# Optimization experiments

Hardware: AMD Instinct MI355X
Metric: run time of the kernel (lower is better)

The kernel has to match this reference:

```python
import jax, jax.numpy as jnp
import numpy as np

N_NODES = 50000
N_EDGES = 800000
IN_CH = 128
HEADS = 2
OUT_CH = 64


def setup_inputs() -> dict:
    key = jax.random.key(0)
    k1, k2, k3, k4, k5 = jax.random.split(key, 5)
    x = jax.random.normal(k1, (N_NODES, IN_CH), dtype=jnp.float32)
    W = jax.random.normal(k2, (IN_CH, HEADS * OUT_CH), dtype=jnp.float32) / np.sqrt(IN_CH)
    att_src = jax.random.normal(k3, (HEADS, OUT_CH), dtype=jnp.float32) / np.sqrt(OUT_CH)
    att_dst = jax.random.normal(k4, (HEADS, OUT_CH), dtype=jnp.float32) / np.sqrt(OUT_CH)
    bias = jnp.zeros((OUT_CH,), dtype=jnp.float32)
    edge_index = jax.random.randint(k5, (2, N_EDGES), 0, N_NODES, dtype=jnp.int64)
    return {"x": x, "W": W, "att_src": att_src, "att_dst": att_dst,
            "bias": bias, "edge_index": edge_index}


def reference(x, W, att_src, att_dst, bias, edge_index):
    # PyG GATConv forward (heads=2, concat=False, add_self_loops=True,
    # negative_slope=0.2, bias on mean-over-heads output).
    N = x.shape[0]
    H, C = att_src.shape
    h = (x @ W).reshape(N, H, C)                       # [N, H, C] projected features

    loop = jnp.arange(N, dtype=edge_index.dtype)
    src = jnp.concatenate([edge_index[0], loop])        # [E+N] message sources
    dst = jnp.concatenate([edge_index[1], loop])        # [E+N] softmax segments

    # per-node attention halves, then gather scalars per edge
    a_src = jnp.einsum('nhc,hc->nh', h, att_src)        # [N, H]
    a_dst = jnp.einsum('nhc,hc->nh', h, att_dst)        # [N, H]
    e = jax.nn.leaky_relu(a_src[src] + a_dst[dst], 0.2) # [E+N, H]

    # segment-softmax over incoming edges of each destination node
    e_max = jax.ops.segment_max(e, dst, num_segments=N)            # [N, H]
    e_exp = jnp.exp(e - e_max[dst])                                 # [E+N, H]
    denom = jax.ops.segment_sum(e_exp, dst, num_segments=N)         # [N, H] (>0: self-loops)
    alpha = e_exp / denom[dst]                                      # [E+N, H]

    # weighted scatter-add aggregation
    msg = alpha[:, :, None] * h[src]                                # [E+N, H, C]
    out = jax.ops.segment_sum(msg, dst, num_segments=N)             # [N, H, C]
    return out.mean(axis=1) + bias                                  # concat=False -> head mean
```

## Files before the change

### kernel.cpp

```cpp
#include <hip/hip_runtime.h>

#define NN 50000
#define NE 800000
#define ETOT (NE + NN)
#define INCH 128
#define OUTC 64
#define LOG2E 1.44269504088896f
#define NBK 196
#define BCAP 5120
#define EPB 1024
#define BTH 1024

#define OFF_HBUF  0
#define OFF_ASRC  12800000
#define OFF_ADST  13200000
#define OFF_GBC   13600000
#define OFF_BBASE 13601024
#define OFF_OFF   13602048
#define OFF_SRC16 13802052
#define OFF_WPK   15502052
#define OFF_BINB  18902052

typedef __attribute__((ext_vector_type(8))) short short8v;
typedef __attribute__((ext_vector_type(4))) float float4v;
typedef unsigned long long ull;

__device__ __forceinline__ unsigned short f2bf(float f) {
    unsigned u = __float_as_uint(f);
    u += 0x7fffu + ((u >> 16) & 1u);
    return (unsigned short)(u >> 16);
}
__device__ __forceinline__ unsigned packbf(float a, float b) {
    return (unsigned)f2bf(a) | ((unsigned)f2bf(b) << 16);
}

#define PITCH 272
#define XLDS_BYTES (64 * PITCH)
#define WT_OFF XLDS_BYTES
#define SMEM_BYTES (XLDS_BYTES + 128 * PITCH)

__global__ __launch_bounds__(256) void k_proj(const float* __restrict__ x,
                                              const float* __restrict__ W,
                                              const float* __restrict__ att_src,
                                              const float* __restrict__ att_dst,
                                              unsigned* __restrict__ hbuf,
                                              float2* __restrict__ asrc,
                                              float2* __restrict__ adst) {
    __shared__ char smem[SMEM_BYTES];
    const int t = threadIdx.x;
    const int nbase = blockIdx.x * 64;

    {
        const int rl = t >> 2;
        const int q  = t & 3;
        int rg = nbase + rl;
        if (rg >= NN) rg = NN - 1;
        const float4* src = (const float4*)(x + (size_t)rg * INCH + q * 32);
        char* dst = smem + rl * PITCH + q * 64;
#pragma unroll
        for (int i = 0; i < 8; ++i) {
            const float4 v = src[i];
            const unsigned lo = packbf(v.x, v.y);
            const unsigned hi = packbf(v.z, v.w);
            *(ull*)(dst + i * 8) = (ull)lo | ((ull)hi << 32);
        }
    }
    {
        const int c  = t & 127;
        const int kh = t >> 7;
        const float* wcol = W + c;
        char* dst = smem + WT_OFF + c * PITCH + kh * 128;
#pragma unroll
        for (int i = 0; i < 16; ++i) {
            const int k = kh * 64 + i * 4;
            const float w0 = wcol[(size_t)(k + 0) * 128];
            const float w1 = wcol[(size_t)(k + 1) * 128];
            const float w2 = wcol[(size_t)(k + 2) * 128];
            const float w3 = wcol[(size_t)(k + 3) * 128];
            const unsigned lo = packbf(w0, w1);
            const unsigned hi = packbf(w2, w3);
            *(ull*)(dst + i * 8) = (ull)lo | ((ull)hi << 32);
        }
    }
    __syncthreads();

    const int w  = t >> 6;
    const int l  = t & 63;
    const int li = l & 15;
    const int g  = l >> 4;

    const char* xb = smem + (w * 16 + li) * PITCH + g * 16;
    const char* wb = smem + WT_OFF + li * PITCH + g * 16;

    float4v acc[8] = {};
#pragma unroll
    for (int ks = 0; ks < 4; ++ks) {
        const short8v aF = *(const short8v*)(xb + ks * 64);
#pragma unroll
        for (int nt = 0; nt < 8; ++nt) {
            const short8v bF = *(const short8v*)(wb + nt * (16 * PITCH) + ks * 64);
            acc[nt] = __builtin_amdgcn_mfma_f32_16x16x32_bf16(aF, bF, acc[nt], 0, 0, 0);
        }
    }

    float aS0[4], aS1[4], aD0[4], aD1[4];
#pragma unroll
    for (int tt = 0; tt < 4; ++tt) {
        aS0[tt] = att_src[tt * 16 + li];
        aS1[tt] = att_src[64 + tt * 16 + li];
        aD0[tt] = att_dst[tt * 16 + li];
        aD1[tt] = att_dst[64 + tt * 16 + li];
    }
#pragma unroll
    for (int r = 0; r < 4; ++r) {
        const int n = nbase + w * 16 + g * 4 + r;
        const bool valid = (n < NN);
        float ps0 = 0.f, ps1 = 0.f, pd0 = 0.f, pd1 = 0.f;
#pragma unroll
        for (int tt = 0; tt < 4; ++tt) {
            const float h0 = acc[tt][r];
            const float h1 = acc[tt + 4][r];
            if (valid) hbuf[(size_t)n * 64 + tt * 16 + li] = packbf(h0, h1);
            ps0 += h0 * aS0[tt];
            ps1 += h1 * aS1[tt];
            pd0 += h0 * aD0[tt];
            pd1 += h1 * aD1[tt];
        }
#pragma unroll
        for (int m = 1; m <= 8; m <<= 1) {
            ps0 += __shfl_xor(ps0, m);
            ps1 += __shfl_xor(ps1, m);
            pd0 += __shfl_xor(pd0, m);
            pd1 += __shfl_xor(pd1, m);
        }
        if (valid && li == 0) {
            asrc[n] = make_float2(ps0 * LOG2E, ps1 * LOG2E);
            adst[n] = make_float2(pd0 * LOG2E, pd1 * LOG2E);
        }
    }
}

__global__ __launch_bounds__(256) void k_binA(const int* __restrict__ ei,
                                              int* __restrict__ gbc,
                                              unsigned* __restrict__ binb) {
    __shared__ int lcnt[NBK];
    __shared__ int lbase[NBK];
    const int t = threadIdx.x;
    const int e0 = blockIdx.x * EPB;

    for (int i = t; i < NBK; i += 256) lcnt[i] = 0;
    __syncthreads();

    int sr[EPB / 256], dr[EPB / 256];
#pragma unroll
    for (int k = 0; k < EPB / 256; ++k) {
        const int e = e0 + k * 256 + t;
        if (e < ETOT) {
            int s, d;
            if (e < NE) { s = ei[e]; d = ei[NE + e]; }
            else        { s = d = e - NE; }
            sr[k] = s; dr[k] = d;
            atomicAdd(&lcnt[d >> 8], 1);
        } else {
            sr[k] = -1; dr[k] = 0;
        }
    }
    __syncthreads();
    for (int i = t; i < NBK; i += 256) {
        const int c = lcnt[i];
        lbase[i] = c ? atomicAdd(&gbc[i], c) : 0;
        lcnt[i] = 0;
    }
    __syncthreads();
#pragma unroll
    for (int k = 0; k < EPB / 256; ++k) {
        if (sr[k] >= 0) {
            const int b = dr[k] >> 8;
            const int r = lbase[b] + atomicAdd(&lcnt[b], 1);
            if (r < BCAP)
                binb[(size_t)b * BCAP + r] =
                    (unsigned)sr[k] | ((unsigned)(dr[k] & 255) << 16);
        }
    }
}

__global__ __launch_bounds__(256) void k_bscan(const int* __restrict__ gbc,
                                               int* __restrict__ bbase,
                                               int* __restrict__ off_last) {
    const int t = threadIdx.x;
    const int v = (t < NBK) ? gbc[t] : 0;
    int incl = v;
#pragma unroll
    for (int o = 1; o < 64; o <<= 1) {
        int u = __shfl_up(incl, o);
        if ((t & 63) >= o) incl += u;
    }
    __shared__ int ws[4], wsx[4];
    if ((t & 63) == 63) ws[t >> 6] = incl;
    __syncthreads();
    if (t == 0) {
        int r = 0;
#pragma unroll
        for (int i = 0; i < 4; ++i) { wsx[i] = r; r += ws[i]; }
        bbase[NBK] = r;
        off_last[0] = r;
    }
    __syncthreads();
    if (t < NBK) bbase[t] = incl - v + wsx[t >> 6];
}

__global__ __launch_bounds__(BTH) void k_binB(const unsigned* __restrict__ binb,
                                              const int* __restrict__ gbc,
                                              const int* __restrict__ bbase,
                                              const float2* __restrict__ asrc,
                                              const float2* __restrict__ adst,
                                              int* __restrict__ off,
                                              unsigned short* __restrict__ srcs16,
                                              unsigned* __restrict__ wpk) {
    __shared__ int lcnt[256];
    __shared__ int lcur[256];
    __shared__ int ws[4], wsx[4];
    const int b = blockIdx.x;
    const int t = threadIdx.x;
    int n = gbc[b];
    if (n > BCAP) n = BCAP;
    const int base = bbase[b];
    const unsigned* bb = binb + (size_t)b * BCAP;

    if (t < 256) lcnt[t] = 0;
    __syncthreads();

    for (int i = t; i < n; i += BTH)
        atomicAdd(&lcnt[(bb[i] >> 16) & 255], 1);
    __syncthreads();

    int v = 0, incl = 0;
    if (t < 256) {
        v = lcnt[t];
        incl = v;
#pragma unroll
        for (int o = 1; o < 64; o <<= 1) {
            int u = __shfl_up(incl, o);
            if ((t & 63) >= o) incl += u;
        }
        if ((t & 63) == 63) ws[t >> 6] = incl;
    }
    __syncthreads();
    if (t == 0) {
        int r = 0;
#pragma unroll
        for (int i = 0; i < 4; ++i) { wsx[i] = r; r += ws[i]; }
    }
    __syncthreads();
    if (t < 256) {
        const int excl = incl - v + wsx[t >> 6];
        lcur[t] = excl;
        const int nd = b * 256 + t;
        if (nd < NN) off[nd] = base + excl;
    }
    __syncthreads();

    for (int i = t; i < n; i += BTH) {
        const unsigned pk = bb[i];
        const int s    = (int)(pk & 0xffffu);
        const int dlow = (int)((pk >> 16) & 255);
        const int pos  = base + atomicAdd(&lcur[dlow], 1);
        const float2 as = asrc[s];
        const float2 ad = adst[b * 256 + dlow];
        float v0 = as.x + ad.x;
        float v1 = as.y + ad.y;
        v0 = v0 > 0.f ? v0 : 0.2f * v0;
        v1 = v1 > 0.f ? v1 : 0.2f * v1;
        srcs16[pos] = (unsigned short)s;
        wpk[pos] = packbf(exp2f(v0), exp2f(v1));
    }
}

__global__ __launch_bounds__(256) void k_agg(const int* __restrict__ off,
                                             const unsigned short* __restrict__ srcs16,
                                             const unsigned* __restrict__ wpk,
                                             const uint2* __restrict__ hbuf2,
                                             const float2* __restrict__ bias2,
                                             float2* __restrict__ out2) {
    const int wid = (int)((blockIdx.x * 256 + threadIdx.x) >> 6);
    const int lane = threadIdx.x & 63;
    if (wid >= NN) return;
    const int half = lane >> 5;
    const int sl   = lane & 31;
    const int beg = off[wid];
    const int end = off[wid + 1];

    float a0x = 0.f, a1x = 0.f, a0y = 0.f, a1y = 0.f, D0 = 0.f, D1 = 0.f;

#define EDGE(wu, p)                                          \
    {                                                        \
        const float w0 = __uint_as_float((wu) << 16);        \
        const float w1 = __uint_as_float((wu) & 0xffff0000u);\
        a0x += w0 * __uint_as_float((p).x << 16);            \
        a1x += w1 * __uint_as_float((p).x & 0xffff0000u);    \
        a0y += w0 * __uint_as_float((p).y << 16);            \
        a1y += w1 * __uint_as_float((p).y & 0xffff0000u);    \
        D0 += w0;                                            \
        D1 += w1;                                            \
    }

    int i = beg + half;
    while (i + 14 < end) {
        unsigned s[8], w[8];
        uint2 p[8];
#pragma unroll
        for (int j = 0; j < 8; ++j) s[j] = srcs16[i + 2 * j];
#pragma unroll
        for (int j = 0; j < 8; ++j) p[j] = hbuf2[(s[j] << 5) | sl];
#pragma unroll
        for (int j = 0; j < 8; ++j) w[j] = wpk[i + 2 * j];
#pragma unroll
        for (int j = 0; j < 8; ++j) EDGE(w[j], p[j])
        i += 16;
    }
    while (i < end) {
        const unsigned s = srcs16[i];
        const uint2 p = hbuf2[(s << 5) | sl];
        const unsigned w = wpk[i];
        EDGE(w, p)
        i += 2;
    }
#undef EDGE

    a0x += __shfl_xor(a0x, 32);
    a1x += __shfl_xor(a1x, 32);
    a0y += __shfl_xor(a0y, 32);
    a1y += __shfl_xor(a1y, 32);
    D0  += __shfl_xor(D0, 32);
    D1  += __shfl_xor(D1, 32);

    if (half == 0) {
        const float2 bv = bias2[sl];
        out2[(size_t)wid * 32 + sl] =
            make_float2(bv.x + 0.5f * (a0x / D0 + a1x / D1),
                        bv.y + 0.5f * (a0y / D0 + a1y / D1));
    }
}

extern "C" void kernel_launch(void* const* d_in, const int* in_sizes, int n_in,
                              void* d_out, int out_size, void* d_ws, size_t ws_size,
                              hipStream_t stream) {
    const float* x       = (const float*)d_in[0];
    const float* W       = (const float*)d_in[1];
    const float* att_src = (const float*)d_in[2];
    const float* att_dst = (const float*)d_in[3];
    const float* bias    = (const float*)d_in[4];
    const int*   ei      = (const int*)d_in[5];
    float* out = (float*)d_out;

    char* ws = (char*)d_ws;
    unsigned*       hbuf   = (unsigned*)(ws + OFF_HBUF);
    float2*         asrc   = (float2*)(ws + OFF_ASRC);
    float2*         adst   = (float2*)(ws + OFF_ADST);
    int*            gbc    = (int*)(ws + OFF_GBC);
    int*            bbase  = (int*)(ws + OFF_BBASE);
    int*            off    = (int*)(ws + OFF_OFF);
    unsigned short* srcs16 = (unsigned short*)(ws + OFF_SRC16);
    unsigned*       wpk    = (unsigned*)(ws + OFF_WPK);
    unsigned*       binb   = (unsigned*)(ws + OFF_BINB);

    hipMemsetAsync(gbc, 0, 1024, stream);

    k_proj<<<(NN + 63) / 64, 256, 0, stream>>>(x, W, att_src, att_dst, hbuf, asrc, adst);
    k_binA<<<(ETOT + EPB - 1) / EPB, 256, 0, stream>>>(ei, gbc, binb);
    k_bscan<<<1, 256, 0, stream>>>(gbc, bbase, off + NN);
    k_binB<<<NBK, BTH, 0, stream>>>(binb, gbc, bbase, asrc, adst, off, srcs16, wpk);
    k_agg<<<(NN * 64 + 255) / 256, 256, 0, stream>>>(off, srcs16, wpk,
                                                     (const uint2*)hbuf,
                                                     (const float2*)bias,
                                                     (float2*)out);
}
```

Before: 106.3 us.

## Split aggregation into four channel-slice passes over a plane-major feature layout

The projected bf16 feature buffer is stored as four planes of 16 channels each instead of node-major rows. Aggregation now runs as four launches, each handling one 16-channel slice, so the gathered working set per pass (about 3.2 MB) can stay in cache. Each wave processes four edges at a time with 16 lanes per edge. In exchange, the edge indices, weights and offsets are re-read four times, there are more kernel launches, and each gather is only 64 bytes.

Result: slower. 133.9 us (+26.0%).

```diff
diff --git a/kernel.cpp b/kernel.cpp
--- a/kernel.cpp
+++ b/kernel.cpp
@@ -120,7 +120,7 @@
         for (int tt = 0; tt < 4; ++tt) {
             const float h0 = acc[tt][r];
             const float h1 = acc[tt + 4][r];
-            if (valid) hbuf[(size_t)n * 64 + tt * 16 + li] = packbf(h0, h1);
+            if (valid) hbuf[((size_t)tt * NN + n) * 16 + li] = packbf(h0, h1);
             ps0 += h0 * aS0[tt];
             ps1 += h1 * aS1[tt];
             pd0 += h0 * aD0[tt];
@@ -276,70 +276,47 @@
     }
 }
 
-__global__ __launch_bounds__(256) void k_agg(const int* __restrict__ off,
-                                             const unsigned short* __restrict__ srcs16,
-                                             const unsigned* __restrict__ wpk,
-                                             const uint2* __restrict__ hbuf2,
-                                             const float2* __restrict__ bias2,
-                                             float2* __restrict__ out2) {
+__global__ __launch_bounds__(256) void k_aggp(const int* __restrict__ off,
+                                              const unsigned short* __restrict__ srcs16,
+                                              const unsigned* __restrict__ wpk,
+                                              const unsigned* __restrict__ hbufG,
+                                              const float* __restrict__ biasG,
+                                              float* __restrict__ outG) {
     const int wid = (int)((blockIdx.x * 256 + threadIdx.x) >> 6);
     const int lane = threadIdx.x & 63;
     if (wid >= NN) return;
-    const int half = lane >> 5;
-    const int sl   = lane & 31;
+    const int eg = lane >> 4;
+    const int li = lane & 15;
     const int beg = off[wid];
     const int end = off[wid + 1];
 
-    float a0x = 0.f, a1x = 0.f, a0y = 0.f, a1y = 0.f, D0 = 0.f, D1 = 0.f;
-
-#define EDGE(wu, p)                                          \
-    {                                                        \
-        const float w0 = __uint_as_float((wu) << 16);        \
-        const float w1 = __uint_as_float((wu) & 0xffff0000u);\
-        a0x += w0 * __uint_as_float((p).x << 16);            \
-        a1x += w1 * __uint_as_float((p).x & 0xffff0000u);    \
-        a0y += w0 * __uint_as_float((p).y << 16);            \
-        a1y += w1 * __uint_as_float((p).y & 0xffff0000u);    \
-        D0 += w0;                                            \
-        D1 += w1;                                            \
-    }
-
-    int i = beg + half;
-    while (i + 14 < end) {
-        unsigned s[8], w[8];
-        uint2 p[8];
-#pragma unroll
-        for (int j = 0; j < 8; ++j) s[j] = srcs16[i + 2 * j];
-#pragma unroll
-        for (int j = 0; j < 8; ++j) p[j] = hbuf2[(s[j] << 5) | sl];
-#pragma unroll
-        for (int j = 0; j < 8; ++j) w[j] = wpk[i + 2 * j];
-#pragma unroll
-        for (int j = 0; j < 8; ++j) EDGE(w[j], p[j])
-        i += 16;
-    }
-    while (i < end) {
-        const unsigned s = srcs16[i];
-        const uint2 p = hbuf2[(s << 5) | sl];
-        const unsigned w = wpk[i];
-        EDGE(w, p)
-        i += 2;
-    }
-#undef EDGE
-
-    a0x += __shfl_xor(a0x, 32);
-    a1x += __shfl_xor(a1x, 32);
-    a0y += __shfl_xor(a0y, 32);
-    a1y += __shfl_xor(a1y, 32);
-    D0  += __shfl_xor(D0, 32);
-    D1  += __shfl_xor(D1, 32);
-
-    if (half == 0) {
-        const float2 bv = bias2[sl];
-        out2[(size_t)wid * 32 + sl] =
-            make_float2(bv.x + 0.5f * (a0x / D0 + a1x / D1),
-                        bv.y + 0.5f * (a0y / D0 + a1y / D1));
-    }
+    float acc0 = 0.f, acc1 = 0.f, D0 = 0.f, D1 = 0.f;
+
+    for (int i = beg; i < end; i += 16) {
+#pragma unroll
+        for (int j = 0; j < 4; ++j) {
+            const int e  = i + j * 4 + eg;
+            const int ec = e < end ? e : end - 1;
+            const unsigned s  = srcs16[ec];
+            const unsigned wv = wpk[ec];
+            const unsigned pk = hbufG[s * 16 + li];
+            float w0 = __uint_as_float(wv << 16);
+            float w1 = __uint_as_float(wv & 0xffff0000u);
+            if (e >= end) { w0 = 0.f; w1 = 0.f; }
+            acc0 += w0 * __uint_as_float(pk << 16);
+            acc1 += w1 * __uint_as_float(pk & 0xffff0000u);
+            D0 += w0;
+            D1 += w1;
+        }
+    }
+
+    acc0 += __shfl_xor(acc0, 16); acc0 += __shfl_xor(acc0, 32);
+    acc1 += __shfl_xor(acc1, 16); acc1 += __shfl_xor(acc1, 32);
+    D0   += __shfl_xor(D0, 16);   D0   += __shfl_xor(D0, 32);
+    D1   += __shfl_xor(D1, 16);   D1   += __shfl_xor(D1, 32);
+
+    if (lane < 16)
+        outG[(size_t)wid * 64 + li] = biasG[li] + 0.5f * (acc0 / D0 + acc1 / D1);
 }
 
 extern "C" void kernel_launch(void* const* d_in, const int* in_sizes, int n_in,
@@ -370,8 +347,11 @@
     k_binA<<<(ETOT + EPB - 1) / EPB, 256, 0, stream>>>(ei, gbc, binb);
     k_bscan<<<1, 256, 0, stream>>>(gbc, bbase, off + NN);
     k_binB<<<NBK, BTH, 0, stream>>>(binb, gbc, bbase, asrc, adst, off, srcs16, wpk);
-    k_agg<<<(NN * 64 + 255) / 256, 256, 0, stream>>>(off, srcs16, wpk,
-                                                     (const uint2*)hbuf,
-                                                     (const float2*)bias,
-                                                     (float2*)out);
-}
+    for (int p = 0; p < 4; ++p) {
+        k_aggp<<<(NN * 64 + 255) / 256, 256, 0, stream>>>(
+            off, srcs16, wpk,
+            hbuf + (size_t)p * NN * 16,
+            bias + p * 16,
+            out + p * 16);
+    }
+}
```
